# Performance work log

Measured on AMD Instinct MI355X. Metric: run time of the kernel, lower is better.

## Reference

```python
import jax, jax.numpy as jnp
import numpy as np

B, N, D = 4, 4096, 1024
QK = D // 8          # qk_dim_div = 8 -> 128
E = 2 * D            # expand_factor = 2 -> 2048


def setup_inputs() -> dict:
    key = jax.random.key(0)
    k1, k2, k3 = jax.random.split(key, 3)
    x = jax.random.normal(k1, (B, N, D), dtype=jnp.float32)
    # xavier-uniform-like scale for the fused expand / project weights
    expand = jax.random.normal(k2, (D, 2 * QK + 2 * E), dtype=jnp.float32) * np.sqrt(2.0 / (D + 2 * QK + 2 * E)).astype(np.float32)
    project = jax.random.normal(k3, (E, D), dtype=jnp.float32) * np.sqrt(2.0 / (E + D)).astype(np.float32)
    position_bias_mult = jnp.float32(4.0)
    return {"x": x, "expand": expand, "project": project, "position_bias_mult": position_bias_mult}


def _layer_norm(x, eps=1e-5):
    mu = jnp.mean(x, axis=-1, keepdims=True)
    var = jnp.mean(jnp.square(x - mu), axis=-1, keepdims=True)
    return (x - mu) * jax.lax.rsqrt(var + eps)


def reference(x, expand, project, position_bias_mult):
    d = x.shape[-1]
    qk, e = d // 8, 2 * d
    n = x.shape[1]

    nx = _layer_norm(x)
    h = nx @ expand                                    # [B, N, 2*qk + 2*e]
    q = h[..., :qk]
    k = h[..., qk:2 * qk]
    linear = h[..., 2 * qk:2 * qk + e]
    pre_gelu = h[..., 2 * qk + e:]

    gated = linear * jax.nn.gelu(pre_gelu, approximate=False)  # torch F.gelu = exact erf
    local = gated[..., :e - d]                          # [B, N, e-d]
    v = gated[..., e - d:]                              # [B, N, d]

    # learned sigmoid position bias under causal mask
    pos = jnp.arange(n)
    base = (pos[None, :] - pos[:, None]).astype(x.dtype)  # j - i
    causal = pos[None, :] <= pos[:, None]
    mask = jnp.where(causal, jax.nn.sigmoid(base + position_bias_mult), -jnp.inf)

    logits = jnp.einsum('bnq,bmq->bnm', q, k) / np.sqrt(qk).astype(np.float32) + mask
    scores = jax.nn.softmax(logits, axis=-1)            # [B, N, N]
    attn = jnp.einsum('bnm,bmd->bnd', scores, v)         # [B, N, d]

    return x + jnp.concatenate([local, attn], axis=-1) @ project
```

## Files before the change

kernel.cpp:

```cpp
#include <hip/hip_runtime.h>
#include <type_traits>

typedef __bf16 bf16x8 __attribute__((ext_vector_type(8)));
typedef __bf16 bf16x4v __attribute__((ext_vector_type(4)));
typedef float f32x4 __attribute__((ext_vector_type(4)));
typedef unsigned short u16x8 __attribute__((ext_vector_type(8)));
typedef unsigned short u16x4 __attribute__((ext_vector_type(4)));

#define NSEQ 4096
#define DM 1024
#define NBATCH 4

__device__ __forceinline__ unsigned short f2bf(float f) {
  unsigned u = __float_as_uint(f);
  u += 0x7FFFu + ((u >> 16) & 1u);
  return (unsigned short)(u >> 16);
}
__device__ __forceinline__ float bf2f(unsigned short h) {
  return __uint_as_float(((unsigned)h) << 16);
}
__device__ __forceinline__ float gelu_fast(float x) {
  const float y = 1.5957691216057308f * (x + 0.044715f * x * x * x);
  return x / (1.0f + __expf(-y));
}

__device__ __forceinline__ void gload_lds16(const unsigned short* src,
                                            unsigned short* dst) {
  __builtin_amdgcn_global_load_lds(
      (const __attribute__((address_space(1))) unsigned int*)src,
      (__attribute__((address_space(3))) unsigned int*)dst, 16, 0, 0);
}

#define BAR() asm volatile("s_barrier" ::: "memory")
#define VMCNT8() asm volatile("s_waitcnt vmcnt(8)" ::: "memory")
#define VMCNT0() asm volatile("s_waitcnt vmcnt(0)" ::: "memory")

__device__ __forceinline__ int perm_col(int n) {
  if (n < 256) return n;
  int c = n - 256;
  if (c < 2048) return 256 + ((c >> 5) << 6) + (c & 31);
  c -= 2048;
  return 256 + ((c >> 5) << 6) + 32 + (c & 31);
}

__global__ __launch_bounds__(256) void ln_kernel(const float* __restrict__ x,
                                                 unsigned short* __restrict__ nx) {
  const int row = blockIdx.x;
  const int tid = threadIdx.x;
  const float4 v = reinterpret_cast<const float4*>(x + (size_t)row * DM)[tid];
  float s = v.x + v.y + v.z + v.w;
  float q = v.x * v.x + v.y * v.y + v.z * v.z + v.w * v.w;
#pragma unroll
  for (int off = 32; off > 0; off >>= 1) {
    s += __shfl_down(s, off);
    q += __shfl_down(q, off);
  }
  __shared__ float ss[4], sq[4];
  if ((tid & 63) == 0) {
    ss[tid >> 6] = s;
    sq[tid >> 6] = q;
  }
  __syncthreads();
  const float ts = ss[0] + ss[1] + ss[2] + ss[3];
  const float tq = sq[0] + sq[1] + sq[2] + sq[3];
  const float mu = ts * (1.0f / DM);
  const float var = tq * (1.0f / DM) - mu * mu;
  const float rs = rsqrtf(var + 1e-5f);
  u16x4 o;
  o[0] = f2bf((v.x - mu) * rs);
  o[1] = f2bf((v.y - mu) * rs);
  o[2] = f2bf((v.z - mu) * rs);
  o[3] = f2bf((v.w - mu) * rs);
  *reinterpret_cast<u16x4*>(nx + (size_t)row * DM + tid * 4) = o;
}

template <bool PERM>
__global__ __launch_bounds__(256) void tconv_kernel(const float* __restrict__ in,
                                                    unsigned short* __restrict__ out,
                                                    int K, int N) {
  __shared__ unsigned short tile[64][72];
  const int n0 = blockIdx.x * 64;
  const int k0 = blockIdx.y * 64;
  const int tid = threadIdx.x;
  const int lr = tid >> 4, lc = (tid & 15) * 4;
#pragma unroll
  for (int p = 0; p < 4; p++) {
    const int r = lr + p * 16;
    float4 v = *reinterpret_cast<const float4*>(in + (size_t)(k0 + r) * N + n0 + lc);
    tile[r][lc + 0] = f2bf(v.x);
    tile[r][lc + 1] = f2bf(v.y);
    tile[r][lc + 2] = f2bf(v.z);
    tile[r][lc + 3] = f2bf(v.w);
  }
  __syncthreads();
  const int nn = tid >> 2, kkg = (tid & 3) * 16;
  u16x8 o0, o1;
#pragma unroll
  for (int j = 0; j < 8; j++) {
    o0[j] = tile[kkg + j][nn];
    o1[j] = tile[kkg + 8 + j][nn];
  }
  const int orow = PERM ? perm_col(n0 + nn) : (n0 + nn);
  unsigned short* dst = out + (size_t)orow * K + k0 + kkg;
  *reinterpret_cast<u16x8*>(dst) = o0;
  *reinterpret_cast<u16x8*>(dst + 8) = o1;
}

template <int MODE>
__global__ __launch_bounds__(512, 2) void gemm256_kernel(
    const unsigned short* __restrict__ A, int lda,
    const unsigned short* __restrict__ Bt, int ldb, void* __restrict__ Cv,
    void* __restrict__ Cv2, int ldc, int K, int ntn,
    const float* __restrict__ X) {
  __shared__ unsigned short G[65536];
  const int tid = threadIdx.x;
  const int lane = tid & 63;
  const int w = tid >> 6;
  const int lq = lane & 15;
  const int lg = lane >> 4;
  const int wm = w >> 2;
  const int wn = w & 3;
  const int bid = blockIdx.x;
  const int m0 = (bid / ntn) * 256;
  const int n0 = (bid % ntn) * 256;
  const int nk = K >> 6;

  auto AH = [&](int db, int kh) { return G + (db * 2 + kh) * 8192; };
  auto BH = [&](int db, int kh) { return G + 32768 + (db * 2 + kh) * 8192; };

  const int g0 = w * 64 + lane;
  const int rowS = g0 >> 2;
  const int kcS = ((g0 & 3) * 8) ^ (((rowS >> 1) & 3) << 3);
  const unsigned short* Asrc = A + (size_t)(m0 + rowS) * lda + kcS;
  const unsigned short* Bsrc = Bt + (size_t)(n0 + rowS) * ldb + kcS;
  const size_t ldaj = (size_t)128 * lda;
  const size_t ldbj = (size_t)128 * ldb;
  const int dstW = w * 64 * 8;

  auto stageA = [&](int db, int kh, int kt2) {
    if (kt2 < nk) {
      const unsigned short* s = Asrc + (size_t)kt2 * 64 + kh * 32;
      unsigned short* d = AH(db, kh) + dstW;
      gload_lds16(s, d);
      gload_lds16(s + ldaj, d + 4096);
    }
  };
  auto stageB = [&](int db, int kh, int kt2) {
    if (kt2 < nk) {
      const unsigned short* s = Bsrc + (size_t)kt2 * 64 + kh * 32;
      unsigned short* d = BH(db, kh) + dstW;
      gload_lds16(s, d);
      gload_lds16(s + ldbj, d + 4096);
    }
  };

  f32x4 acc[8][4];
#pragma unroll
  for (int i = 0; i < 8; i++)
#pragma unroll
    for (int j = 0; j < 4; j++)
#pragma unroll
      for (int r = 0; r < 4; r++) acc[i][j][r] = 0.0f;

  stageA(0, 0, 0);
  stageB(0, 0, 0);
  stageA(0, 1, 0);
  stageB(0, 1, 0);
  stageA(1, 0, 1);
  stageB(1, 0, 1);
  VMCNT8();
  BAR();

  const int aBase = wm * 128;
  const int bBase = wn * 64;
  const int cSwz = (lg * 8) ^ (((lq >> 1) & 3) << 3);

#pragma unroll 1
  for (int kt = 0; kt < nk; ++kt) {
    const int buf = kt & 1;
    bf16x8 af[4], bf0[4], bf1[4];

#pragma unroll
    for (int i = 0; i < 4; i++)
      af[i] = *reinterpret_cast<const bf16x8*>(
          AH(buf, 0) + (aBase + i * 16 + lq) * 32 + cSwz);
#pragma unroll
    for (int j = 0; j < 4; j++)
      bf0[j] = *reinterpret_cast<const bf16x8*>(
          BH(buf, 0) + (bBase + j * 16 + lq) * 32 + cSwz);
    stageA(buf ^ 1, 1, kt + 1);
    BAR();
    __builtin_amdgcn_s_setprio(1);
#pragma unroll
    for (int i = 0; i < 4; i++)
#pragma unroll
      for (int j = 0; j < 4; j++)
        acc[i][j] =
            __builtin_amdgcn_mfma_f32_16x16x32_bf16(af[i], bf0[j], acc[i][j], 0, 0, 0);
    __builtin_amdgcn_s_setprio(0);
    BAR();

#pragma unroll
    for (int i = 0; i < 4; i++)
      af[i] = *reinterpret_cast<const bf16x8*>(
          AH(buf, 0) + (aBase + 64 + i * 16 + lq) * 32 + cSwz);
    stageB(buf ^ 1, 1, kt + 1);
    VMCNT8();
    BAR();
    __builtin_amdgcn_s_setprio(1);
#pragma unroll
    for (int i = 0; i < 4; i++)
#pragma unroll
      for (int j = 0; j < 4; j++)
        acc[4 + i][j] = __builtin_amdgcn_mfma_f32_16x16x32_bf16(af[i], bf0[j],
                                                                acc[4 + i][j], 0, 0, 0);
    __builtin_amdgcn_s_setprio(0);
    BAR();

#pragma unroll
    for (int i = 0; i < 4; i++)
      af[i] = *reinterpret_cast<const bf16x8*>(
          AH(buf, 1) + (aBase + i * 16 + lq) * 32 + cSwz);
#pragma unroll
    for (int j = 0; j < 4; j++)
      bf1[j] = *reinterpret_cast<const bf16x8*>(
          BH(buf, 1) + (bBase + j * 16 + lq) * 32 + cSwz);
    stageA(buf, 0, kt + 2);
    BAR();
    __builtin_amdgcn_s_setprio(1);
#pragma unroll
    for (int i = 0; i < 4; i++)
#pragma unroll
      for (int j = 0; j < 4; j++)
        acc[i][j] =
            __builtin_amdgcn_mfma_f32_16x16x32_bf16(af[i], bf1[j], acc[i][j], 0, 0, 0);
    __builtin_amdgcn_s_setprio(0);
    BAR();

#pragma unroll
    for (int i = 0; i < 4; i++)
      af[i] = *reinterpret_cast<const bf16x8*>(
          AH(buf, 1) + (aBase + 64 + i * 16 + lq) * 32 + cSwz);
    stageB(buf, 0, kt + 2);
    VMCNT8();
    BAR();
    __builtin_amdgcn_s_setprio(1);
#pragma unroll
    for (int i = 0; i < 4; i++)
#pragma unroll
      for (int j = 0; j < 4; j++)
        acc[4 + i][j] = __builtin_amdgcn_mfma_f32_16x16x32_bf16(af[i], bf1[j],
                                                                acc[4 + i][j], 0, 0, 0);
    __builtin_amdgcn_s_setprio(0);
    BAR();
  }

  if (MODE == 1) {
    float* C = reinterpret_cast<float*>(Cv);
#pragma unroll
    for (int I = 0; I < 8; I++)
#pragma unroll
      for (int j = 0; j < 4; j++)
#pragma unroll
        for (int r = 0; r < 4; r++) {
          const int row = m0 + wm * 128 + I * 16 + lg * 4 + r;
          const int col = n0 + wn * 64 + j * 16 + lq;
          const size_t off = (size_t)row * ldc + col;
          C[off] = X[off] + acc[I][j][r];
        }
  } else {
    VMCNT0();
    BAR();
    unsigned short* concat = reinterpret_cast<unsigned short*>(Cv);
    unsigned short* vT = reinterpret_cast<unsigned short*>(Cv2);
    if (n0 < 2048) {
      const int c0 = n0 >> 1;
#pragma unroll
      for (int I = 0; I < 8; I++)
#pragma unroll
        for (int j = 0; j < 2; j++)
#pragma unroll
          for (int r = 0; r < 4; r++) {
            const float g = acc[I][j][r] * gelu_fast(acc[I][j + 2][r]);
            G[(wm * 128 + I * 16 + lg * 4 + r) * 136 + wn * 32 + j * 16 + lq] =
                f2bf(g);
          }
      BAR();
#pragma unroll
      for (int it = 0; it < 8; ++it) {
        const int chunk = tid + it * 512;
        const int row = chunk >> 4, cc = chunk & 15;
        *reinterpret_cast<u16x8*>(concat + (size_t)(m0 + row) * 2048 + c0 +
                                  cc * 8) =
            *reinterpret_cast<const u16x8*>(&G[row * 136 + cc * 8]);
      }
    } else {
      const int d0 = (n0 >> 1) - 1024;
      const int b = m0 >> 12;
      const int nn0 = m0 & 4095;
#pragma unroll
      for (int I = 0; I < 8; I++)
#pragma unroll
        for (int j = 0; j < 2; j++)
#pragma unroll
          for (int r = 0; r < 4; r++) {
            const float g = acc[I][j][r] * gelu_fast(acc[I][j + 2][r]);
            G[(wn * 32 + j * 16 + lq) * 264 + wm * 128 + I * 16 + lg * 4 + r] =
                f2bf(g);
          }
      BAR();
#pragma unroll
      for (int it = 0; it < 8; ++it) {
        const int chunk = tid + it * 512;
        const int d = chunk >> 5, cc = chunk & 31;
        *reinterpret_cast<u16x8*>(vT + (size_t)(b * 1024 + d0 + d) * 4096 +
                                  nn0 + cc * 8) =
            *reinterpret_cast<const u16x8*>(&G[d * 264 + cc * 8]);
      }
    }
  }
}

__global__ __launch_bounds__(256, 4) void qk_kernel(
    const unsigned short* __restrict__ nx, const unsigned short* __restrict__ eT,
    unsigned short* __restrict__ qk) {
  __shared__ unsigned short As[128][64];
  __shared__ unsigned short Bs[128][64];
  const int tid = threadIdx.x;
  const int m0 = (blockIdx.x >> 1) * 128;
  const int n0 = (blockIdx.x & 1) * 128;
  const int lane = tid & 63;
  const int w = tid >> 6;
  const int lr = lane & 15;
  const int lg = lane >> 4;
  const int wr = (w >> 1) * 64;
  const int wc = (w & 1) * 64;
  const int rSwz = (lr & 7) << 3;

  f32x4 acc[4][4];
#pragma unroll
  for (int i = 0; i < 4; i++)
#pragma unroll
    for (int j = 0; j < 4; j++)
#pragma unroll
      for (int r = 0; r < 4; r++) acc[i][j][r] = 0.0f;

  for (int k0 = 0; k0 < 1024; k0 += 64) {
#pragma unroll
    for (int j = 0; j < 4; j++) {
      const int boff = w * 4096 + j * 1024 + lane * 16;
      const int row = boff >> 7;
      const int col = (((boff & 127) >> 1)) ^ ((row & 7) << 3);
      gload_lds16(nx + (size_t)(m0 + row) * DM + k0 + col,
                  &As[0][0] + (boff - lane * 16) / 2);
    }
#pragma unroll
    for (int j = 0; j < 4; j++) {
      const int boff = w * 4096 + j * 1024 + lane * 16;
      const int row = boff >> 7;
      const int col = (((boff & 127) >> 1)) ^ ((row & 7) << 3);
      gload_lds16(eT + (size_t)(n0 + row) * DM + k0 + col,
                  &Bs[0][0] + (boff - lane * 16) / 2);
    }
    __syncthreads();
#pragma unroll
    for (int kk = 0; kk < 64; kk += 32) {
      bf16x8 af[4], bfr[4];
#pragma unroll
      for (int i = 0; i < 4; i++)
        af[i] = *reinterpret_cast<const bf16x8*>(
            &As[wr + i * 16 + lr][(kk + lg * 8) ^ rSwz]);
#pragma unroll
      for (int j = 0; j < 4; j++)
        bfr[j] = *reinterpret_cast<const bf16x8*>(
            &Bs[wc + j * 16 + lr][(kk + lg * 8) ^ rSwz]);
#pragma unroll
      for (int i = 0; i < 4; i++)
#pragma unroll
        for (int j = 0; j < 4; j++)
          acc[i][j] = __builtin_amdgcn_mfma_f32_16x16x32_bf16(af[i], bfr[j],
                                                              acc[i][j], 0, 0, 0);
    }
    __syncthreads();
  }

#pragma unroll
  for (int i = 0; i < 4; i++)
#pragma unroll
    for (int j = 0; j < 4; j++)
#pragma unroll
      for (int r = 0; r < 4; r++) {
        const int row = m0 + wr + i * 16 + lg * 4 + r;
        const int col = n0 + wc + j * 16 + lr;
        qk[(size_t)row * 256 + col] = f2bf(acc[i][j][r]);
      }
}

#define P_TILE 16384
#define P_PER_B 8650752
__global__ __launch_bounds__(512, 4) void pk_kernel(
    const unsigned short* __restrict__ qk, const float* __restrict__ pbm_ptr,
    unsigned short* __restrict__ P, float* __restrict__ l) {
  __shared__ unsigned short Ks[128][136];
  const int tid = threadIdx.x;
  const int lane = tid & 63;
  const int w = tid >> 6;
  const int lq = lane & 15;
  const int lg = lane >> 4;
  const int bid = blockIdx.x;
  const int b = bid / 528;
  const int t = bid - b * 528;
  int qt = (int)((sqrtf((float)(8 * t + 1)) - 1.0f) * 0.5f);
  while ((qt + 1) * (qt + 2) / 2 <= t) ++qt;
  while (qt * (qt + 1) / 2 > t) --qt;
  const int kt = t - qt * (qt + 1) / 2;
  const float pbm = *pbm_ptr;
  const float SCALE = 0.08838834764831845f;

  const unsigned short* qb = qk + (size_t)b * NSEQ * 256;

#pragma unroll
  for (int p = 0; p < 4; p++) {
    const int task = tid + p * 512;
    const int row = task >> 4;
    const int ch = task & 15;
    bf16x8 v = *reinterpret_cast<const bf16x8*>(
        qb + (size_t)(kt * 128 + row) * 256 + 128 + ch * 8);
    *reinterpret_cast<bf16x8*>(&Ks[row][ch * 8]) = v;
  }
  const int qloc = w * 16 + lq;
  bf16x8 qf[4];
#pragma unroll
  for (int ks = 0; ks < 4; ks++)
    qf[ks] = *reinterpret_cast<const bf16x8*>(
        qb + (size_t)(qt * 128 + qloc) * 256 + ks * 32 + lg * 8);
  __syncthreads();

  f32x4 sa[8];
#pragma unroll
  for (int sub = 0; sub < 8; sub++)
#pragma unroll
    for (int r = 0; r < 4; r++) sa[sub][r] = 0.0f;
#pragma unroll
  for (int ks = 0; ks < 4; ks++)
#pragma unroll
    for (int sub = 0; sub < 8; sub++) {
      bf16x8 kf =
          *reinterpret_cast<const bf16x8*>(&Ks[sub * 16 + lq][ks * 32 + lg * 8]);
      sa[sub] = __builtin_amdgcn_mfma_f32_16x16x32_bf16(kf, qf[ks], sa[sub], 0, 0, 0);
    }
  const size_t KL = (size_t)(qt + 1) * 128;
  unsigned short* Prow = P + (size_t)b * P_PER_B +
                         (size_t)(qt * (qt + 1) / 2) * P_TILE + (size_t)qloc * KL +
                         kt * 128;
  float ps = 0.0f;
  const bool diag = (kt == qt);
#pragma unroll
  for (int sub = 0; sub < 8; sub++) {
    bf16x4v pv;
#pragma unroll
    for (int r = 0; r < 4; r++) {
      const int kvloc = sub * 16 + lg * 4 + r;
      float p;
      if (diag && kvloc > qloc) {
        p = 0.0f;
      } else {
        const float dn = (float)((kt - qt) * 128 + kvloc - qloc) + pbm;
        const float s = sa[sub][r] * SCALE + 1.0f / (1.0f + __expf(-dn));
        p = __expf(s);
      }
      ps += p;
      pv[r] = (__bf16)p;
    }
    *reinterpret_cast<bf16x4v*>(Prow + sub * 16 + lg * 4) = pv;
  }
  ps += __shfl_xor(ps, 16);
  ps += __shfl_xor(ps, 32);
  if (lane < 16) atomicAdd(&l[b * NSEQ + qt * 128 + w * 16 + lane], ps);
}

__global__ __launch_bounds__(256, 4) void pv_kernel(
    const unsigned short* __restrict__ P, const unsigned short* __restrict__ vT,
    const float* __restrict__ l, unsigned short* __restrict__ concat) {
  __shared__ unsigned short LDSp[17408];
  unsigned short* Asb = LDSp;
  unsigned short* Bsb = LDSp + 8192;
  const int tid = threadIdx.x;
  const int bid = blockIdx.x;
  const int qt = 31 - (bid >> 5);
  const int rest = bid & 31;
  const int b = rest >> 3;
  const int nt = rest & 7;
  const int KL = (qt + 1) * 128;
  const unsigned short* A =
      P + (size_t)b * P_PER_B + (size_t)(qt * (qt + 1) / 2) * P_TILE;
  const unsigned short* Bt = vT + (size_t)b * DM * NSEQ;
  const int n0 = nt * 128;
  const int lane = tid & 63;
  const int w = tid >> 6;
  const int lr = lane & 15;
  const int lg = lane >> 4;
  const int wr = (w >> 1) * 64;
  const int wc = (w & 1) * 64;
  const int rSwz = (lr & 7) << 3;

  f32x4 acc[4][4];
#pragma unroll
  for (int i = 0; i < 4; i++)
#pragma unroll
    for (int j = 0; j < 4; j++)
#pragma unroll
      for (int r = 0; r < 4; r++) acc[i][j][r] = 0.0f;

  for (int k0 = 0; k0 < KL; k0 += 64) {
#pragma unroll
    for (int j = 0; j < 4; j++) {
      const int boff = w * 4096 + j * 1024 + lane * 16;
      const int row = boff >> 7;
      const int col = (((boff & 127) >> 1)) ^ ((row & 7) << 3);
      gload_lds16(A + (size_t)row * KL + k0 + col,
                  Asb + (boff - lane * 16) / 2);
    }
#pragma unroll
    for (int j = 0; j < 4; j++) {
      const int boff = w * 4096 + j * 1024 + lane * 16;
      const int row = boff >> 7;
      const int col = (((boff & 127) >> 1)) ^ ((row & 7) << 3);
      gload_lds16(Bt + (size_t)(n0 + row) * NSEQ + k0 + col,
                  Bsb + (boff - lane * 16) / 2);
    }
    __syncthreads();
#pragma unroll
    for (int kk = 0; kk < 64; kk += 32) {
      bf16x8 af[4], bfr[4];
#pragma unroll
      for (int i = 0; i < 4; i++)
        af[i] = *reinterpret_cast<const bf16x8*>(
            Asb + (wr + i * 16 + lr) * 64 + ((kk + lg * 8) ^ rSwz));
#pragma unroll
      for (int j = 0; j < 4; j++)
        bfr[j] = *reinterpret_cast<const bf16x8*>(
            Bsb + (wc + j * 16 + lr) * 64 + ((kk + lg * 8) ^ rSwz));
#pragma unroll
      for (int i = 0; i < 4; i++)
#pragma unroll
        for (int j = 0; j < 4; j++)
          acc[i][j] = __builtin_amdgcn_mfma_f32_16x16x32_bf16(af[i], bfr[j],
                                                              acc[i][j], 0, 0, 0);
    }
    __syncthreads();
  }

  const float* lb = l + b * NSEQ + qt * 128;
#pragma unroll
  for (int i = 0; i < 4; i++) {
    f32x4 lv = *reinterpret_cast<const f32x4*>(&lb[wr + i * 16 + lg * 4]);
    f32x4 inv;
#pragma unroll
    for (int r = 0; r < 4; r++) inv[r] = 1.0f / lv[r];
#pragma unroll
    for (int j = 0; j < 4; j++)
#pragma unroll
      for (int r = 0; r < 4; r++)
        LDSp[(wr + i * 16 + lg * 4 + r) * 136 + wc + j * 16 + lr] =
            f2bf(acc[i][j][r] * inv[r]);
  }
  __syncthreads();
#pragma unroll
  for (int it = 0; it < 8; ++it) {
    const int chunk = tid + it * 256;
    const int row = chunk >> 4, cc = chunk & 15;
    *reinterpret_cast<u16x8*>(concat +
                              (size_t)(b * NSEQ + qt * 128 + row) * 2048 + 1024 +
                              n0 + cc * 8) =
        *reinterpret_cast<const u16x8*>(&LDSp[row * 136 + cc * 8]);
  }
}

extern "C" void kernel_launch(void* const* d_in, const int* in_sizes, int n_in,
                              void* d_out, int out_size, void* d_ws,
                              size_t ws_size, hipStream_t stream) {
  (void)in_sizes;
  (void)n_in;
  (void)out_size;
  const float* x = (const float*)d_in[0];
  const float* expand = (const float*)d_in[1];
  const float* project = (const float*)d_in[2];
  const float* pbm = (const float*)d_in[3];
  float* out = (float*)d_out;

  const size_t QK_BYTES = (size_t)16384 * 256 * 2;
  const size_t VT_BYTES = (size_t)16384 * 1024 * 2;
  const size_t P_BYTES = (size_t)NBATCH * P_PER_B * 2;
  const size_t L_BYTES = (size_t)NBATCH * NSEQ * 4;
  const size_t GH_BYTES = (size_t)16384 * 4096 * 2;
  const size_t CAT_BYTES = (size_t)16384 * 2048 * 2;
  const size_t NX_BYTES = (size_t)16384 * DM * 2;
  if (ws_size < QK_BYTES + GH_BYTES + CAT_BYTES + NX_BYTES) return;

  char* ws = (char*)d_ws;
  unsigned short* qk = (unsigned short*)ws;
  unsigned short* vT = (unsigned short*)(ws + QK_BYTES);
  unsigned short* P = (unsigned short*)(ws + QK_BYTES + VT_BYTES);
  float* l = (float*)(ws + QK_BYTES + VT_BYTES + P_BYTES);
  unsigned short* expandT =
      (unsigned short*)(ws + QK_BYTES + VT_BYTES + P_BYTES + L_BYTES);
  unsigned short* concat = (unsigned short*)(ws + QK_BYTES + GH_BYTES);
  unsigned short* nx = (unsigned short*)(ws + QK_BYTES + GH_BYTES + CAT_BYTES);
  unsigned short* projectT = nx;

  tconv_kernel<true><<<dim3(68, 16), 256, 0, stream>>>(expand, expandT, 1024, 4352);
  ln_kernel<<<16384, 256, 0, stream>>>(x, nx);
  qk_kernel<<<dim3(256), 256, 0, stream>>>(nx, expandT, qk);
  gemm256_kernel<2><<<dim3(64 * 16), 512, 0, stream>>>(
      nx, DM, expandT + (size_t)256 * DM, DM, (void*)concat, (void*)vT, 0, DM,
      16, nullptr);
  hipMemsetAsync(l, 0, L_BYTES, stream);
  pk_kernel<<<dim3(NBATCH * 528), 512, 0, stream>>>(qk, pbm, P, l);
  pv_kernel<<<dim3(1024), 256, 0, stream>>>(P, vT, l, concat);
  tconv_kernel<false><<<dim3(16, 32), 256, 0, stream>>>(project, projectT, 2048, DM);
  gemm256_kernel<1><<<dim3(64 * 4), 512, 0, stream>>>(
      concat, 2048, projectT, 2048, (void*)out, nullptr, DM, 2048, 4, x);
}
```

Baseline: 428.6 us.

## Fold QK projection into expand GEMM and reorder PV tile scheduling

Removes the separate qk_kernel launch. The q/k projection becomes an extra 256-wide column tile of the big expand GEMM, scheduled first and written straight to the qk buffer. It also changes the pv_kernel query-tile order from strictly heaviest-first to a mixed heavy/light interleave, aiming to balance causal workload across CUs. This trades one launch and a low-occupancy small GEMM for 64 extra blocks in the big GEMM, and the new PV order may hurt tail balance.

```diff
diff --git a/kernel.cpp b/kernel.cpp
--- a/kernel.cpp
+++ b/kernel.cpp
@@ -110,7 +110,7 @@
 __global__ __launch_bounds__(512, 2) void gemm256_kernel(
     const unsigned short* __restrict__ A, int lda,
     const unsigned short* __restrict__ Bt, int ldb, void* __restrict__ Cv,
-    void* __restrict__ Cv2, int ldc, int K, int ntn,
+    void* __restrict__ Cv2, void* __restrict__ Cv3, int ldc, int K, int ntn,
     const float* __restrict__ X) {
   __shared__ unsigned short G[65536];
   const int tid = threadIdx.x;
@@ -121,8 +121,19 @@
   const int wm = w >> 2;
   const int wn = w & 3;
   const int bid = blockIdx.x;
-  const int m0 = (bid / ntn) * 256;
-  const int n0 = (bid % ntn) * 256;
+  int m0, n0;
+  if (MODE == 2) {
+    if (bid < 64) {
+      m0 = bid * 256;
+      n0 = 0;
+    } else {
+      m0 = ((bid - 64) >> 4) * 256;
+      n0 = (1 + ((bid - 64) & 15)) * 256;
+    }
+  } else {
+    m0 = (bid / ntn) * 256;
+    n0 = (bid % ntn) * 256;
+  }
   const int nk = K >> 6;
 
   auto AH = [&](int db, int kh) { return G + (db * 2 + kh) * 8192; };
@@ -273,8 +284,20 @@
     BAR();
     unsigned short* concat = reinterpret_cast<unsigned short*>(Cv);
     unsigned short* vT = reinterpret_cast<unsigned short*>(Cv2);
-    if (n0 < 2048) {
-      const int c0 = n0 >> 1;
+    if (n0 == 0) {
+      unsigned short* qkp = reinterpret_cast<unsigned short*>(Cv3);
+#pragma unroll
+      for (int I = 0; I < 8; I++)
+#pragma unroll
+        for (int j = 0; j < 4; j++)
+#pragma unroll
+          for (int r = 0; r < 4; r++) {
+            const int row = m0 + wm * 128 + I * 16 + lg * 4 + r;
+            const int col = wn * 64 + j * 16 + lq;
+            qkp[(size_t)row * 256 + col] = f2bf(acc[I][j][r]);
+          }
+    } else if (n0 < 2304) {
+      const int c0 = (n0 - 256) >> 1;
 #pragma unroll
       for (int I = 0; I < 8; I++)
 #pragma unroll
@@ -295,7 +318,7 @@
             *reinterpret_cast<const u16x8*>(&G[row * 136 + cc * 8]);
       }
     } else {
-      const int d0 = (n0 >> 1) - 1024;
+      const int d0 = ((n0 - 256) >> 1) - 1024;
       const int b = m0 >> 12;
       const int nn0 = m0 & 4095;
 #pragma unroll
@@ -319,81 +342,6 @@
       }
     }
   }
-}
-
-__global__ __launch_bounds__(256, 4) void qk_kernel(
-    const unsigned short* __restrict__ nx, const unsigned short* __restrict__ eT,
-    unsigned short* __restrict__ qk) {
-  __shared__ unsigned short As[128][64];
-  __shared__ unsigned short Bs[128][64];
-  const int tid = threadIdx.x;
-  const int m0 = (blockIdx.x >> 1) * 128;
-  const int n0 = (blockIdx.x & 1) * 128;
-  const int lane = tid & 63;
-  const int w = tid >> 6;
-  const int lr = lane & 15;
-  const int lg = lane >> 4;
-  const int wr = (w >> 1) * 64;
-  const int wc = (w & 1) * 64;
-  const int rSwz = (lr & 7) << 3;
-
-  f32x4 acc[4][4];
-#pragma unroll
-  for (int i = 0; i < 4; i++)
-#pragma unroll
-    for (int j = 0; j < 4; j++)
-#pragma unroll
-      for (int r = 0; r < 4; r++) acc[i][j][r] = 0.0f;
-
-  for (int k0 = 0; k0 < 1024; k0 += 64) {
-#pragma unroll
-    for (int j = 0; j < 4; j++) {
-      const int boff = w * 4096 + j * 1024 + lane * 16;
-      const int row = boff >> 7;
-      const int col = (((boff & 127) >> 1)) ^ ((row & 7) << 3);
-      gload_lds16(nx + (size_t)(m0 + row) * DM + k0 + col,
-                  &As[0][0] + (boff - lane * 16) / 2);
-    }
-#pragma unroll
-    for (int j = 0; j < 4; j++) {
-      const int boff = w * 4096 + j * 1024 + lane * 16;
-      const int row = boff >> 7;
-      const int col = (((boff & 127) >> 1)) ^ ((row & 7) << 3);
-      gload_lds16(eT + (size_t)(n0 + row) * DM + k0 + col,
-                  &Bs[0][0] + (boff - lane * 16) / 2);
-    }
-    __syncthreads();
-#pragma unroll
-    for (int kk = 0; kk < 64; kk += 32) {
-      bf16x8 af[4], bfr[4];
-#pragma unroll
-      for (int i = 0; i < 4; i++)
-        af[i] = *reinterpret_cast<const bf16x8*>(
-            &As[wr + i * 16 + lr][(kk + lg * 8) ^ rSwz]);
-#pragma unroll
-      for (int j = 0; j < 4; j++)
-        bfr[j] = *reinterpret_cast<const bf16x8*>(
-            &Bs[wc + j * 16 + lr][(kk + lg * 8) ^ rSwz]);
-#pragma unroll
-      for (int i = 0; i < 4; i++)
-#pragma unroll
-        for (int j = 0; j < 4; j++)
-          acc[i][j] = __builtin_amdgcn_mfma_f32_16x16x32_bf16(af[i], bfr[j],
-                                                              acc[i][j], 0, 0, 0);
-    }
-    __syncthreads();
-  }
-
-#pragma unroll
-  for (int i = 0; i < 4; i++)
-#pragma unroll
-    for (int j = 0; j < 4; j++)
-#pragma unroll
-      for (int r = 0; r < 4; r++) {
-        const int row = m0 + wr + i * 16 + lg * 4 + r;
-        const int col = n0 + wc + j * 16 + lr;
-        qk[(size_t)row * 256 + col] = f2bf(acc[i][j][r]);
-      }
 }
 
 #define P_TILE 16384
@@ -487,7 +435,12 @@
   unsigned short* Bsb = LDSp + 8192;
   const int tid = threadIdx.x;
   const int bid = blockIdx.x;
-  const int qt = 31 - (bid >> 5);
+  const int g = bid >> 5;
+  int qt;
+  if (g < 8) qt = 31 - g;
+  else if (g < 16) qt = 23 - g;
+  else if (g < 24) qt = g;
+  else qt = g - 24;
   const int rest = bid & 31;
   const int b = rest >> 3;
   const int nt = rest & 7;
@@ -611,14 +564,13 @@
 
   tconv_kernel<true><<<dim3(68, 16), 256, 0, stream>>>(expand, expandT, 1024, 4352);
   ln_kernel<<<16384, 256, 0, stream>>>(x, nx);
-  qk_kernel<<<dim3(256), 256, 0, stream>>>(nx, expandT, qk);
-  gemm256_kernel<2><<<dim3(64 * 16), 512, 0, stream>>>(
-      nx, DM, expandT + (size_t)256 * DM, DM, (void*)concat, (void*)vT, 0, DM,
-      16, nullptr);
+  gemm256_kernel<2><<<dim3(1088), 512, 0, stream>>>(
+      nx, DM, expandT, DM, (void*)concat, (void*)vT, (void*)qk, 0, DM, 17,
+      nullptr);
   hipMemsetAsync(l, 0, L_BYTES, stream);
   pk_kernel<<<dim3(NBATCH * 528), 512, 0, stream>>>(qk, pbm, P, l);
   pv_kernel<<<dim3(1024), 256, 0, stream>>>(P, vT, l, concat);
   tconv_kernel<false><<<dim3(16, 32), 256, 0, stream>>>(project, projectT, 2048, DM);
   gemm256_kernel<1><<<dim3(64 * 4), 512, 0, stream>>>(
-      concat, 2048, projectT, 2048, (void*)out, nullptr, DM, 2048, 4, x);
-}
+      concat, 2048, projectT, 2048, (void*)out, nullptr, nullptr, DM, 2048, 4, x);
+}
```

After: 422.4 us. About the same (-1.4%).

## Replace atomic row-sum accumulation with per-tile partials and rebalance PV tile order

Applied to the files above, without the earlier changes.

pk_kernel now writes each key-tile's partial row sums to a 2D buffer instead of doing atomicAdd into a zeroed array. pv_kernel reduces those partials into shared memory at start, which removes the memset and the atomics. PV block-to-query-tile mapping is reordered to interleave heavy and light tiles, and the project transpose is moved earlier into its own buffer. The cost is an extra serial reduction over up to 32 partials per row in pv_kernel.

```diff
diff --git a/kernel.cpp b/kernel.cpp
--- a/kernel.cpp
+++ b/kernel.cpp
@@ -400,7 +400,7 @@
 #define P_PER_B 8650752
 __global__ __launch_bounds__(512, 4) void pk_kernel(
     const unsigned short* __restrict__ qk, const float* __restrict__ pbm_ptr,
-    unsigned short* __restrict__ P, float* __restrict__ l) {
+    unsigned short* __restrict__ P, float* __restrict__ l2d) {
   __shared__ unsigned short Ks[128][136];
   const int tid = threadIdx.x;
   const int lane = tid & 63;
@@ -476,18 +476,25 @@
   }
   ps += __shfl_xor(ps, 16);
   ps += __shfl_xor(ps, 32);
-  if (lane < 16) atomicAdd(&l[b * NSEQ + qt * 128 + w * 16 + lane], ps);
+  if (lane < 16)
+    l2d[(((size_t)b * 32 + qt) * 32 + kt) * 128 + w * 16 + lane] = ps;
 }
 
 __global__ __launch_bounds__(256, 4) void pv_kernel(
     const unsigned short* __restrict__ P, const unsigned short* __restrict__ vT,
-    const float* __restrict__ l, unsigned short* __restrict__ concat) {
+    const float* __restrict__ l2d, unsigned short* __restrict__ concat) {
   __shared__ unsigned short LDSp[17408];
+  __shared__ float lrow[128];
   unsigned short* Asb = LDSp;
   unsigned short* Bsb = LDSp + 8192;
   const int tid = threadIdx.x;
   const int bid = blockIdx.x;
-  const int qt = 31 - (bid >> 5);
+  const int g = bid >> 5;
+  int qt;
+  if (g < 8) qt = 31 - g;
+  else if (g < 16) qt = 23 - g;
+  else if (g < 24) qt = g;
+  else qt = g - 24;
   const int rest = bid & 31;
   const int b = rest >> 3;
   const int nt = rest & 7;
@@ -504,6 +511,13 @@
   const int wc = (w & 1) * 64;
   const int rSwz = (lr & 7) << 3;
 
+  if (tid < 128) {
+    const float* base = l2d + (((size_t)b * 32 + qt) * 32) * 128 + tid;
+    float s = 0.0f;
+    for (int kt = 0; kt <= qt; ++kt) s += base[kt * 128];
+    lrow[tid] = 1.0f / s;
+  }
+
   f32x4 acc[4][4];
 #pragma unroll
   for (int i = 0; i < 4; i++)
@@ -551,13 +565,9 @@
     __syncthreads();
   }
 
-  const float* lb = l + b * NSEQ + qt * 128;
 #pragma unroll
   for (int i = 0; i < 4; i++) {
-    f32x4 lv = *reinterpret_cast<const f32x4*>(&lb[wr + i * 16 + lg * 4]);
-    f32x4 inv;
-#pragma unroll
-    for (int r = 0; r < 4; r++) inv[r] = 1.0f / lv[r];
+    f32x4 inv = *reinterpret_cast<const f32x4*>(&lrow[wr + i * 16 + lg * 4]);
 #pragma unroll
     for (int j = 0; j < 4; j++)
 #pragma unroll
@@ -592,7 +602,7 @@
   const size_t QK_BYTES = (size_t)16384 * 256 * 2;
   const size_t VT_BYTES = (size_t)16384 * 1024 * 2;
   const size_t P_BYTES = (size_t)NBATCH * P_PER_B * 2;
-  const size_t L_BYTES = (size_t)NBATCH * NSEQ * 4;
+  const size_t L2D_BYTES = (size_t)NBATCH * 32 * 32 * 128 * 4;
   const size_t GH_BYTES = (size_t)16384 * 4096 * 2;
   const size_t CAT_BYTES = (size_t)16384 * 2048 * 2;
   const size_t NX_BYTES = (size_t)16384 * DM * 2;
@@ -602,23 +612,24 @@
   unsigned short* qk = (unsigned short*)ws;
   unsigned short* vT = (unsigned short*)(ws + QK_BYTES);
   unsigned short* P = (unsigned short*)(ws + QK_BYTES + VT_BYTES);
-  float* l = (float*)(ws + QK_BYTES + VT_BYTES + P_BYTES);
+  float* l2d = (float*)(ws + QK_BYTES + VT_BYTES + P_BYTES);
   unsigned short* expandT =
-      (unsigned short*)(ws + QK_BYTES + VT_BYTES + P_BYTES + L_BYTES);
+      (unsigned short*)(ws + QK_BYTES + VT_BYTES + P_BYTES + L2D_BYTES);
+  unsigned short* projectT =
+      (unsigned short*)(ws + QK_BYTES + VT_BYTES + P_BYTES + L2D_BYTES +
+                        (size_t)4352 * 1024 * 2);
   unsigned short* concat = (unsigned short*)(ws + QK_BYTES + GH_BYTES);
   unsigned short* nx = (unsigned short*)(ws + QK_BYTES + GH_BYTES + CAT_BYTES);
-  unsigned short* projectT = nx;
 
   tconv_kernel<true><<<dim3(68, 16), 256, 0, stream>>>(expand, expandT, 1024, 4352);
+  tconv_kernel<false><<<dim3(16, 32), 256, 0, stream>>>(project, projectT, 2048, DM);
   ln_kernel<<<16384, 256, 0, stream>>>(x, nx);
   qk_kernel<<<dim3(256), 256, 0, stream>>>(nx, expandT, qk);
   gemm256_kernel<2><<<dim3(64 * 16), 512, 0, stream>>>(
       nx, DM, expandT + (size_t)256 * DM, DM, (void*)concat, (void*)vT, 0, DM,
       16, nullptr);
-  hipMemsetAsync(l, 0, L_BYTES, stream);
-  pk_kernel<<<dim3(NBATCH * 528), 512, 0, stream>>>(qk, pbm, P, l);
-  pv_kernel<<<dim3(1024), 256, 0, stream>>>(P, vT, l, concat);
-  tconv_kernel<false><<<dim3(16, 32), 256, 0, stream>>>(project, projectT, 2048, DM);
+  pk_kernel<<<dim3(NBATCH * 528), 512, 0, stream>>>(qk, pbm, P, l2d);
+  pv_kernel<<<dim3(1024), 256, 0, stream>>>(P, vT, l2d, concat);
   gemm256_kernel<1><<<dim3(64 * 4), 512, 0, stream>>>(
       concat, 2048, projectT, 2048, (void*)out, nullptr, DM, 2048, 4, x);
 }
```

Measured after the change: 432.9 us, median of 3. About the same (+1.0%).
